# Performance work log

Hardware: AMD Instinct MI355X
Metric: run time of the kernel (lower is better)

Reference implementation:

```python
import jax, jax.numpy as jnp
import numpy as np

N_NODES = 100000
N_EDGES = 1600000
D_IN = 128
D_HID = 128
D_OUT = 128


def setup_inputs() -> dict:
    key = jax.random.key(0)
    ks = jax.random.split(key, 12)
    x = jax.random.normal(ks[0], (N_NODES, D_IN), dtype=jnp.float32)
    edge_index = jax.random.randint(ks[1], (2, N_EDGES), 0, N_NODES, dtype=jnp.int64)
    s = 0.05
    # GraphConv layer l: out = agg @ w_rel + x @ w_root + b  (lin_rel has bias, lin_root does not)
    w_rel1 = jax.random.normal(ks[2], (D_IN, D_HID), dtype=jnp.float32) * s
    w_root1 = jax.random.normal(ks[3], (D_IN, D_HID), dtype=jnp.float32) * s
    b1 = jax.random.normal(ks[4], (D_HID,), dtype=jnp.float32) * s
    w_rel2 = jax.random.normal(ks[5], (D_HID, D_HID), dtype=jnp.float32) * s
    w_root2 = jax.random.normal(ks[6], (D_HID, D_HID), dtype=jnp.float32) * s
    b2 = jax.random.normal(ks[7], (D_HID,), dtype=jnp.float32) * s
    w_rel3 = jax.random.normal(ks[8], (D_HID, D_OUT), dtype=jnp.float32) * s
    w_root3 = jax.random.normal(ks[9], (D_HID, D_OUT), dtype=jnp.float32) * s
    b3 = jax.random.normal(ks[10], (D_OUT,), dtype=jnp.float32) * s
    return {"x": x, "edge_index": edge_index,
            "w_rel1": w_rel1, "w_root1": w_root1, "b1": b1,
            "w_rel2": w_rel2, "w_root2": w_root2, "b2": b2,
            "w_rel3": w_rel3, "w_root3": w_root3, "b3": b3}


def _graph_conv(h, src, dst, w_rel, w_root, b):
    # sum-aggregate neighbor features (message = x_j, flow src -> dst),
    # then linear; identical math to PyG GraphConv with aggr='add'.
    agg = jax.ops.segment_sum(h[src], dst, num_segments=h.shape[0])
    return agg @ w_rel + h @ w_root + b


def reference(x, edge_index, w_rel1, w_root1, b1, w_rel2, w_root2, b2, w_rel3, w_root3, b3):
    src, dst = edge_index[0], edge_index[1]
    h = jax.nn.relu(_graph_conv(x, src, dst, w_rel1, w_root1, b1))
    h = jax.nn.relu(_graph_conv(h, src, dst, w_rel2, w_root2, b2))
    out = _graph_conv(h, src, dst, w_rel3, w_root3, b3)
    return out
```

## Files before the change

### kernel.cpp

```cpp
#include <hip/hip_runtime.h>
#include <hip/hip_bf16.h>
#include <stdint.h>

typedef __hip_bfloat16 bf16;
typedef __hip_bfloat162 bf162;

typedef __attribute__((ext_vector_type(8))) short short8;
typedef __attribute__((ext_vector_type(4))) float floatx4;

#define BSH   8
#define BSZ   256
#define CHUNK 8192
#define NBMAX 512


__device__ __forceinline__ float2 load2f(const bf16* __restrict__ p) {
    const unsigned int u = *(const unsigned int*)p;
    return make_float2(__uint_as_float((u & 0xffffu) << 16),
                       __uint_as_float(u & 0xffff0000u));
}


__global__ __launch_bounds__(256)
void cvt_kernel(const float* __restrict__ x, bf16* __restrict__ y, int n4) {
    int i = blockIdx.x * 256 + threadIdx.x;
    if (i < n4) {
        float4 v = ((const float4*)x)[i];
        bf162 a, b;
        a.x = __float2bfloat16(v.x); a.y = __float2bfloat16(v.y);
        b.x = __float2bfloat16(v.z); b.y = __float2bfloat16(v.w);
        ((bf162*)y)[i * 2]     = a;
        ((bf162*)y)[i * 2 + 1] = b;
    }
}

__global__ __launch_bounds__(256)
void prep_w_kernel(const float* __restrict__ wrel, const float* __restrict__ wroot,
                   bf16* __restrict__ wsw) {
    int t = blockIdx.x * 256 + threadIdx.x;
    if (t >= 4096) return;
    const int lane = t & 63;
    const int ct   = (t >> 6) & 7;
    const int kt   = t >> 9;
    const int kbase = kt * 32 + (lane >> 4) * 8;
    const int n     = ct * 16 + (lane & 15);
    bf16* q = wsw + (size_t)t * 8;
#pragma unroll
    for (int j = 0; j < 8; ++j) {
        const int k = kbase + j;
        const float v = (k < 128) ? wrel[k * 128 + n] : wroot[(k - 128) * 128 + n];
        q[j] = __float2bfloat16(v);
    }
}


__global__ __launch_bounds__(256)
void bhist_kernel(const int* __restrict__ dst, int* __restrict__ T,
                  int E, int NB, int GB) {
    __shared__ int lh[NBMAX];
    const int b = blockIdx.x;
    for (int u = threadIdx.x; u < NB; u += 256) lh[u] = 0;
    __syncthreads();
    const int beg = b * CHUNK, end = min(beg + CHUNK, E);
    for (int e = beg + threadIdx.x; e < end; e += 256)
        atomicAdd(&lh[dst[e] >> BSH], 1);
    __syncthreads();
    for (int u = threadIdx.x; u < NB; u += 256)
        T[u * GB + b] = lh[u];
}

__global__ __launch_bounds__(256)
void scan1_kernel(const int* __restrict__ deg, int* __restrict__ rp,
                  int* __restrict__ bsum, int n) {
    __shared__ int s[256];
    const int tid = threadIdx.x;
    const int i = blockIdx.x * 256 + tid;
    const int d = (i < n) ? deg[i] : 0;
    s[tid] = d;
    __syncthreads();
    for (int off = 1; off < 256; off <<= 1) {
        int u = (tid >= off) ? s[tid - off] : 0;
        __syncthreads();
        s[tid] += u;
        __syncthreads();
    }
    if (i < n) rp[i] = s[tid] - d;
    if (tid == 255) bsum[blockIdx.x] = s[255];
}

__global__ __launch_bounds__(512)
void scan2_kernel(int* __restrict__ bsum, int G) {
    __shared__ int s[512];
    const int tid = threadIdx.x;
    const int d = (tid < G) ? bsum[tid] : 0;
    s[tid] = d;
    __syncthreads();
    for (int off = 1; off < 512; off <<= 1) {
        int u = (tid >= off) ? s[tid - off] : 0;
        __syncthreads();
        s[tid] += u;
        __syncthreads();
    }
    if (tid < G) bsum[tid] = s[tid] - d;
}

__global__ __launch_bounds__(256)
void scan3_kernel(int* __restrict__ rp, const int* __restrict__ bsum, int n) {
    const int i = blockIdx.x * 256 + threadIdx.x;
    if (i < n) rp[i] += bsum[blockIdx.x];
}

__global__ __launch_bounds__(256)
void bscatter_kernel(const int* __restrict__ src, const int* __restrict__ dst,
                     const int* __restrict__ T, int* __restrict__ ebuf,
                     int E, int NB, int GB) {
    __shared__ int lofs[NBMAX];
    const int b = blockIdx.x;
    for (int u = threadIdx.x; u < NB; u += 256)
        lofs[u] = T[u * GB + b];
    __syncthreads();
    const int beg = b * CHUNK, end = min(beg + CHUNK, E);
    for (int e = beg + threadIdx.x; e < end; e += 256) {
        const int d = dst[e];
        const int u = d >> BSH;
        const int pos = atomicAdd(&lofs[u], 1);
        ebuf[pos] = (src[e] << BSH) | (d & (BSZ - 1));
    }
}

__global__ __launch_bounds__(256)
void bbuild_kernel(const int* __restrict__ T, const int* __restrict__ ebuf,
                   int* __restrict__ rp, int* __restrict__ col,
                   int E, int N, int NB, int GB) {
    __shared__ int s[256];
    __shared__ int lrank[256];
    const int u = blockIdx.x;
    const int tid = threadIdx.x;
    const int beg = T[u * GB];
    const int end = (u + 1 < NB) ? T[(u + 1) * GB] : E;

    lrank[tid] = 0;
    __syncthreads();
    for (int e = beg + tid; e < end; e += 256)
        atomicAdd(&lrank[ebuf[e] & (BSZ - 1)], 1);
    __syncthreads();
    const int cntv = lrank[tid];
    s[tid] = cntv;
    __syncthreads();
    for (int off = 1; off < 256; off <<= 1) {
        int v = (tid >= off) ? s[tid - off] : 0;
        __syncthreads();
        s[tid] += v;
        __syncthreads();
    }
    const int excl = s[tid] - cntv;
    const int node = u * BSZ + tid;
    if (node < N) rp[node] = beg + excl;
    if (u == NB - 1 && tid == 0) rp[N] = E;
    lrank[tid] = beg + excl;
    __syncthreads();
    for (int e = beg + tid; e < end; e += 256) {
        const int p = ebuf[e];
        const int pos = atomicAdd(&lrank[p & (BSZ - 1)], 1);
        col[pos] = p >> BSH;
    }
}


__global__ __launch_bounds__(256)
void agg_kernel(const bf16* __restrict__ h, const int* __restrict__ rp,
                const int* __restrict__ col, bf16* __restrict__ agg, int N) {
    const int lane = threadIdx.x & 63;
    const int wid  = threadIdx.x >> 6;
    const int node = blockIdx.x * 4 + wid;
    if (node >= N) return;
    const int beg = rp[node], end = rp[node + 1];
    const int f = lane * 2;
    float2 acc = make_float2(0.f, 0.f);
    int e = beg;
    for (; e + 8 <= end; e += 8) {
        const int s0 = col[e],     s1 = col[e + 1], s2 = col[e + 2], s3 = col[e + 3];
        const int s4 = col[e + 4], s5 = col[e + 5], s6 = col[e + 6], s7 = col[e + 7];
        const float2 a0 = load2f(h + (size_t)s0 * 128 + f);
        const float2 a1 = load2f(h + (size_t)s1 * 128 + f);
        const float2 a2 = load2f(h + (size_t)s2 * 128 + f);
        const float2 a3 = load2f(h + (size_t)s3 * 128 + f);
        const float2 a4 = load2f(h + (size_t)s4 * 128 + f);
        const float2 a5 = load2f(h + (size_t)s5 * 128 + f);
        const float2 a6 = load2f(h + (size_t)s6 * 128 + f);
        const float2 a7 = load2f(h + (size_t)s7 * 128 + f);
        acc.x += ((a0.x + a1.x) + (a2.x + a3.x)) + ((a4.x + a5.x) + (a6.x + a7.x));
        acc.y += ((a0.y + a1.y) + (a2.y + a3.y)) + ((a4.y + a5.y) + (a6.y + a7.y));
    }
    for (; e + 2 <= end; e += 2) {
        const int s0 = col[e], s1 = col[e + 1];
        const float2 a0 = load2f(h + (size_t)s0 * 128 + f);
        const float2 a1 = load2f(h + (size_t)s1 * 128 + f);
        acc.x += a0.x + a1.x;
        acc.y += a0.y + a1.y;
    }
    if (e < end) {
        const float2 a0 = load2f(h + (size_t)col[e] * 128 + f);
        acc.x += a0.x;
        acc.y += a0.y;
    }
    bf162 o;
    o.x = __float2bfloat16(acc.x);
    o.y = __float2bfloat16(acc.y);
    *(bf162*)(agg + (size_t)node * 128 + f) = o;
}


template <bool RELU, typename OT>
__global__ __launch_bounds__(256)
void mfma_gemm_kernel(const bf16* __restrict__ Aagg, const bf16* __restrict__ Hroot,
                      const bf16* __restrict__ wsw, const float* __restrict__ bias,
                      OT* __restrict__ out, int M) {
    const int tid  = threadIdx.x;
    const int lane = tid & 63;
    const int wave = tid >> 6;
    const int l15  = lane & 15;
    const int quad = lane >> 4;

    const int row_a = blockIdx.x * 64 + wave * 16 + l15;
    const bool rowok = row_a < M;

    floatx4 acc[8];
#pragma unroll
    for (int ct = 0; ct < 8; ++ct) acc[ct] = (floatx4){0.f, 0.f, 0.f, 0.f};

#pragma unroll
    for (int kt = 0; kt < 8; ++kt) {
        const bf16* Abase = (kt < 4) ? Aagg : Hroot;
        const int k0 = (kt & 3) * 32 + quad * 8;
        short8 afrag = (short8){0, 0, 0, 0, 0, 0, 0, 0};
        if (rowok) afrag = *(const short8*)(Abase + (size_t)row_a * 128 + k0);
#pragma unroll
        for (int ct = 0; ct < 8; ++ct) {
            const short8 bfrag = *(const short8*)(wsw + (size_t)((kt * 8 + ct) * 64 + lane) * 8);
            acc[ct] = __builtin_amdgcn_mfma_f32_16x16x32_bf16(afrag, bfrag, acc[ct], 0, 0, 0);
        }
    }

    const int row_o = blockIdx.x * 64 + wave * 16 + quad * 4;
#pragma unroll
    for (int ct = 0; ct < 8; ++ct) {
        const int colc = ct * 16 + l15;
        const float bv = bias[colc];
#pragma unroll
        for (int r = 0; r < 4; ++r) {
            const int row = row_o + r;
            if (row < M) {
                float v = acc[ct][r] + bv;
                if (RELU) v = fmaxf(v, 0.f);
                if constexpr (sizeof(OT) == 2)
                    ((bf16*)out)[(size_t)row * 128 + colc] = __float2bfloat16(v);
                else
                    ((float*)out)[(size_t)row * 128 + colc] = v;
            }
        }
    }
}


extern "C" void kernel_launch(void* const* d_in, const int* in_sizes, int n_in,
                              void* d_out, int out_size, void* d_ws, size_t ws_size,
                              hipStream_t stream) {
    const float* x       = (const float*)d_in[0];
    const int*   ei      = (const int*)d_in[1];
    const float* w_rel1  = (const float*)d_in[2];
    const float* w_root1 = (const float*)d_in[3];
    const float* b1      = (const float*)d_in[4];
    const float* w_rel2  = (const float*)d_in[5];
    const float* w_root2 = (const float*)d_in[6];
    const float* b2      = (const float*)d_in[7];
    const float* w_rel3  = (const float*)d_in[8];
    const float* w_root3 = (const float*)d_in[9];
    const float* b3      = (const float*)d_in[10];
    float* out = (float*)d_out;

    const int N = in_sizes[0] / 128;
    const int E = in_sizes[1] / 2;
    const int* src = ei;
    const int* dst = ei + E;

    char* w = (char*)d_ws;
    auto alloc = [&](size_t bytes) {
        char* p = w;
        w += (bytes + 255) & ~(size_t)255;
        return p;
    };
    int*  col  = (int*)alloc((size_t)E * 4);
    int*  rp   = (int*)alloc((size_t)(N + 1) * 4);
    bf16* h1   = (bf16*)alloc((size_t)N * 128 * 2);
    bf16* xbf  = (bf16*)alloc((size_t)N * 128 * 2);
    bf16* agg  = (bf16*)alloc((size_t)N * 128 * 2);
    bf16* wsw1 = (bf16*)alloc(32768 * 2);
    bf16* wsw2 = (bf16*)alloc(32768 * 2);
    bf16* wsw3 = (bf16*)alloc(32768 * 2);
    bf16* h2   = xbf;
    int*  T    = (int*)h1;
    int*  bsum = (int*)(h1 + 1024 * 1024);
    int*  ebuf = (int*)agg;

    const int NB = (N + BSZ - 1) / BSZ;
    const int GB = (E + CHUNK - 1) / CHUNK;
    const int nT = NB * GB;
    const int scanTBlocks = (nT + 255) / 256;

    const int aggBlocks  = (N + 3) / 4;
    const int gemmBlocks = (N + 63) / 64;
    const int cvtBlocks  = (N * 32 + 255) / 256;

    cvt_kernel<<<cvtBlocks, 256, 0, stream>>>(x, xbf, N * 32);
    prep_w_kernel<<<16, 256, 0, stream>>>(w_rel1, w_root1, wsw1);
    prep_w_kernel<<<16, 256, 0, stream>>>(w_rel2, w_root2, wsw2);
    prep_w_kernel<<<16, 256, 0, stream>>>(w_rel3, w_root3, wsw3);

    bhist_kernel<<<GB, 256, 0, stream>>>(dst, T, E, NB, GB);
    scan1_kernel<<<scanTBlocks, 256, 0, stream>>>(T, T, bsum, nT);
    scan2_kernel<<<1, 512, 0, stream>>>(bsum, scanTBlocks);
    scan3_kernel<<<scanTBlocks, 256, 0, stream>>>(T, bsum, nT);
    bscatter_kernel<<<GB, 256, 0, stream>>>(src, dst, T, ebuf, E, NB, GB);
    bbuild_kernel<<<NB, 256, 0, stream>>>(T, ebuf, rp, col, E, N, NB, GB);

    agg_kernel<<<aggBlocks, 256, 0, stream>>>(xbf, rp, col, agg, N);
    mfma_gemm_kernel<true, bf16><<<gemmBlocks, 256, 0, stream>>>(agg, xbf, wsw1, b1, h1, N);
    agg_kernel<<<aggBlocks, 256, 0, stream>>>(h1, rp, col, agg, N);
    mfma_gemm_kernel<true, bf16><<<gemmBlocks, 256, 0, stream>>>(agg, h1, wsw2, b2, h2, N);
    agg_kernel<<<aggBlocks, 256, 0, stream>>>(h2, rp, col, agg, N);
    mfma_gemm_kernel<false, float><<<gemmBlocks, 256, 0, stream>>>(agg, h2, wsw3, b3, out, N);
}
```

Before: 483.6 us.

## Fuse neighbor aggregation into MFMA GEMM via shared-memory tile per layer

Each GraphConv layer now gathers and sums neighbor rows for its 64-node tile straight into shared memory, then runs the MFMA GEMM from that tile and the root features. This removes the intermediate aggregation buffer write and read and three kernel launches. The weight and input conversion kernels are merged into one launch. Each wave now processes 16 nodes serially, which reduces the number of concurrent gathers in flight and the number of blocks.

```diff
diff --git a/kernel.cpp b/kernel.cpp
--- a/kernel.cpp
+++ b/kernel.cpp
@@ -20,25 +20,31 @@
                        __uint_as_float(u & 0xffff0000u));
 }
 
-
-__global__ __launch_bounds__(256)
-void cvt_kernel(const float* __restrict__ x, bf16* __restrict__ y, int n4) {
-    int i = blockIdx.x * 256 + threadIdx.x;
-    if (i < n4) {
-        float4 v = ((const float4*)x)[i];
-        bf162 a, b;
-        a.x = __float2bfloat16(v.x); a.y = __float2bfloat16(v.y);
-        b.x = __float2bfloat16(v.z); b.y = __float2bfloat16(v.w);
-        ((bf162*)y)[i * 2]     = a;
-        ((bf162*)y)[i * 2 + 1] = b;
-    }
-}
-
-__global__ __launch_bounds__(256)
-void prep_w_kernel(const float* __restrict__ wrel, const float* __restrict__ wroot,
-                   bf16* __restrict__ wsw) {
-    int t = blockIdx.x * 256 + threadIdx.x;
-    if (t >= 4096) return;
+__global__ __launch_bounds__(256)
+void prep_kernel(const float* __restrict__ x, bf16* __restrict__ y, int n4, int nCvt,
+                 const float* __restrict__ wr1, const float* __restrict__ wo1,
+                 const float* __restrict__ wr2, const float* __restrict__ wo2,
+                 const float* __restrict__ wr3, const float* __restrict__ wo3,
+                 bf16* __restrict__ w1, bf16* __restrict__ w2, bf16* __restrict__ w3) {
+    const int b = blockIdx.x;
+    if (b < nCvt) {
+        const int i = b * 256 + threadIdx.x;
+        if (i < n4) {
+            float4 v = ((const float4*)x)[i];
+            bf162 a, c;
+            a.x = __float2bfloat16(v.x); a.y = __float2bfloat16(v.y);
+            c.x = __float2bfloat16(v.z); c.y = __float2bfloat16(v.w);
+            ((bf162*)y)[i * 2]     = a;
+            ((bf162*)y)[i * 2 + 1] = c;
+        }
+        return;
+    }
+    int t = (b - nCvt) * 256 + threadIdx.x;
+    const int layer = t >> 12;
+    t &= 4095;
+    const float* wrel  = (layer == 0) ? wr1 : (layer == 1) ? wr2 : wr3;
+    const float* wroot = (layer == 0) ? wo1 : (layer == 1) ? wo2 : wo3;
+    bf16*        wsw   = (layer == 0) ? w1  : (layer == 1) ? w2  : w3;
     const int lane = t & 63;
     const int ct   = (t >> 6) & 7;
     const int kt   = t >> 9;
@@ -167,62 +173,62 @@
 }
 
 
-__global__ __launch_bounds__(256)
-void agg_kernel(const bf16* __restrict__ h, const int* __restrict__ rp,
-                const int* __restrict__ col, bf16* __restrict__ agg, int N) {
-    const int lane = threadIdx.x & 63;
-    const int wid  = threadIdx.x >> 6;
-    const int node = blockIdx.x * 4 + wid;
-    if (node >= N) return;
-    const int beg = rp[node], end = rp[node + 1];
-    const int f = lane * 2;
-    float2 acc = make_float2(0.f, 0.f);
-    int e = beg;
-    for (; e + 8 <= end; e += 8) {
-        const int s0 = col[e],     s1 = col[e + 1], s2 = col[e + 2], s3 = col[e + 3];
-        const int s4 = col[e + 4], s5 = col[e + 5], s6 = col[e + 6], s7 = col[e + 7];
-        const float2 a0 = load2f(h + (size_t)s0 * 128 + f);
-        const float2 a1 = load2f(h + (size_t)s1 * 128 + f);
-        const float2 a2 = load2f(h + (size_t)s2 * 128 + f);
-        const float2 a3 = load2f(h + (size_t)s3 * 128 + f);
-        const float2 a4 = load2f(h + (size_t)s4 * 128 + f);
-        const float2 a5 = load2f(h + (size_t)s5 * 128 + f);
-        const float2 a6 = load2f(h + (size_t)s6 * 128 + f);
-        const float2 a7 = load2f(h + (size_t)s7 * 128 + f);
-        acc.x += ((a0.x + a1.x) + (a2.x + a3.x)) + ((a4.x + a5.x) + (a6.x + a7.x));
-        acc.y += ((a0.y + a1.y) + (a2.y + a3.y)) + ((a4.y + a5.y) + (a6.y + a7.y));
-    }
-    for (; e + 2 <= end; e += 2) {
-        const int s0 = col[e], s1 = col[e + 1];
-        const float2 a0 = load2f(h + (size_t)s0 * 128 + f);
-        const float2 a1 = load2f(h + (size_t)s1 * 128 + f);
-        acc.x += a0.x + a1.x;
-        acc.y += a0.y + a1.y;
-    }
-    if (e < end) {
-        const float2 a0 = load2f(h + (size_t)col[e] * 128 + f);
-        acc.x += a0.x;
-        acc.y += a0.y;
-    }
-    bf162 o;
-    o.x = __float2bfloat16(acc.x);
-    o.y = __float2bfloat16(acc.y);
-    *(bf162*)(agg + (size_t)node * 128 + f) = o;
-}
-
-
 template <bool RELU, typename OT>
 __global__ __launch_bounds__(256)
-void mfma_gemm_kernel(const bf16* __restrict__ Aagg, const bf16* __restrict__ Hroot,
-                      const bf16* __restrict__ wsw, const float* __restrict__ bias,
-                      OT* __restrict__ out, int M) {
+void fused_layer_kernel(const bf16* __restrict__ H, const int* __restrict__ rp,
+                        const int* __restrict__ col, const bf16* __restrict__ wsw,
+                        const float* __restrict__ bias, OT* __restrict__ out, int M) {
+    __shared__ __align__(16) bf16 atile[64][136];
+
     const int tid  = threadIdx.x;
     const int lane = tid & 63;
     const int wave = tid >> 6;
     const int l15  = lane & 15;
     const int quad = lane >> 4;
-
-    const int row_a = blockIdx.x * 64 + wave * 16 + l15;
+    const int base = blockIdx.x * 64;
+
+    const int f = lane * 2;
+#pragma unroll 1
+    for (int i = 0; i < 16; ++i) {
+        const int node = base + wave * 16 + i;
+        float2 acc = make_float2(0.f, 0.f);
+        if (node < M) {
+            const int beg = rp[node], end = rp[node + 1];
+            int e = beg;
+            for (; e + 8 <= end; e += 8) {
+                const int s0 = col[e],     s1 = col[e + 1], s2 = col[e + 2], s3 = col[e + 3];
+                const int s4 = col[e + 4], s5 = col[e + 5], s6 = col[e + 6], s7 = col[e + 7];
+                const float2 a0 = load2f(H + (size_t)s0 * 128 + f);
+                const float2 a1 = load2f(H + (size_t)s1 * 128 + f);
+                const float2 a2 = load2f(H + (size_t)s2 * 128 + f);
+                const float2 a3 = load2f(H + (size_t)s3 * 128 + f);
+                const float2 a4 = load2f(H + (size_t)s4 * 128 + f);
+                const float2 a5 = load2f(H + (size_t)s5 * 128 + f);
+                const float2 a6 = load2f(H + (size_t)s6 * 128 + f);
+                const float2 a7 = load2f(H + (size_t)s7 * 128 + f);
+                acc.x += ((a0.x + a1.x) + (a2.x + a3.x)) + ((a4.x + a5.x) + (a6.x + a7.x));
+                acc.y += ((a0.y + a1.y) + (a2.y + a3.y)) + ((a4.y + a5.y) + (a6.y + a7.y));
+            }
+            for (; e + 2 <= end; e += 2) {
+                const int s0 = col[e], s1 = col[e + 1];
+                const float2 a0 = load2f(H + (size_t)s0 * 128 + f);
+                const float2 a1 = load2f(H + (size_t)s1 * 128 + f);
+                acc.x += a0.x + a1.x;
+                acc.y += a0.y + a1.y;
+            }
+            if (e < end) {
+                const float2 a0 = load2f(H + (size_t)col[e] * 128 + f);
+                acc.x += a0.x;
+                acc.y += a0.y;
+            }
+        }
+        bf162 o;
+        o.x = __float2bfloat16(acc.x);
+        o.y = __float2bfloat16(acc.y);
+        *(bf162*)&atile[wave * 16 + i][f] = o;
+    }
+
+    const int row_a = base + wave * 16 + l15;
     const bool rowok = row_a < M;
 
     floatx4 acc[8];
@@ -231,10 +237,14 @@
 
 #pragma unroll
     for (int kt = 0; kt < 8; ++kt) {
-        const bf16* Abase = (kt < 4) ? Aagg : Hroot;
         const int k0 = (kt & 3) * 32 + quad * 8;
-        short8 afrag = (short8){0, 0, 0, 0, 0, 0, 0, 0};
-        if (rowok) afrag = *(const short8*)(Abase + (size_t)row_a * 128 + k0);
+        short8 afrag;
+        if (kt < 4) {
+            afrag = *(const short8*)&atile[wave * 16 + l15][k0];
+        } else {
+            afrag = (short8){0, 0, 0, 0, 0, 0, 0, 0};
+            if (rowok) afrag = *(const short8*)(H + (size_t)row_a * 128 + k0);
+        }
 #pragma unroll
         for (int ct = 0; ct < 8; ++ct) {
             const short8 bfrag = *(const short8*)(wsw + (size_t)((kt * 8 + ct) * 64 + lane) * 8);
@@ -242,7 +252,7 @@
         }
     }
 
-    const int row_o = blockIdx.x * 64 + wave * 16 + quad * 4;
+    const int row_o = base + wave * 16 + quad * 4;
 #pragma unroll
     for (int ct = 0; ct < 8; ++ct) {
         const int colc = ct * 16 + l15;
@@ -294,28 +304,26 @@
     int*  rp   = (int*)alloc((size_t)(N + 1) * 4);
     bf16* h1   = (bf16*)alloc((size_t)N * 128 * 2);
     bf16* xbf  = (bf16*)alloc((size_t)N * 128 * 2);
-    bf16* agg  = (bf16*)alloc((size_t)N * 128 * 2);
+    int*  ebuf = (int*)alloc((size_t)E * 4);
     bf16* wsw1 = (bf16*)alloc(32768 * 2);
     bf16* wsw2 = (bf16*)alloc(32768 * 2);
     bf16* wsw3 = (bf16*)alloc(32768 * 2);
     bf16* h2   = xbf;
     int*  T    = (int*)h1;
     int*  bsum = (int*)(h1 + 1024 * 1024);
-    int*  ebuf = (int*)agg;
 
     const int NB = (N + BSZ - 1) / BSZ;
     const int GB = (E + CHUNK - 1) / CHUNK;
     const int nT = NB * GB;
     const int scanTBlocks = (nT + 255) / 256;
 
-    const int aggBlocks  = (N + 3) / 4;
-    const int gemmBlocks = (N + 63) / 64;
-    const int cvtBlocks  = (N * 32 + 255) / 256;
-
-    cvt_kernel<<<cvtBlocks, 256, 0, stream>>>(x, xbf, N * 32);
-    prep_w_kernel<<<16, 256, 0, stream>>>(w_rel1, w_root1, wsw1);
-    prep_w_kernel<<<16, 256, 0, stream>>>(w_rel2, w_root2, wsw2);
-    prep_w_kernel<<<16, 256, 0, stream>>>(w_rel3, w_root3, wsw3);
+    const int fusedBlocks = (N + 63) / 64;
+    const int cvtBlocks   = (N * 32 + 255) / 256;
+
+    prep_kernel<<<cvtBlocks + 48, 256, 0, stream>>>(
+        x, xbf, N * 32, cvtBlocks,
+        w_rel1, w_root1, w_rel2, w_root2, w_rel3, w_root3,
+        wsw1, wsw2, wsw3);
 
     bhist_kernel<<<GB, 256, 0, stream>>>(dst, T, E, NB, GB);
     scan1_kernel<<<scanTBlocks, 256, 0, stream>>>(T, T, bsum, nT);
@@ -324,10 +332,7 @@
     bscatter_kernel<<<GB, 256, 0, stream>>>(src, dst, T, ebuf, E, NB, GB);
     bbuild_kernel<<<NB, 256, 0, stream>>>(T, ebuf, rp, col, E, N, NB, GB);
 
-    agg_kernel<<<aggBlocks, 256, 0, stream>>>(xbf, rp, col, agg, N);
-    mfma_gemm_kernel<true, bf16><<<gemmBlocks, 256, 0, stream>>>(agg, xbf, wsw1, b1, h1, N);
-    agg_kernel<<<aggBlocks, 256, 0, stream>>>(h1, rp, col, agg, N);
-    mfma_gemm_kernel<true, bf16><<<gemmBlocks, 256, 0, stream>>>(agg, h1, wsw2, b2, h2, N);
-    agg_kernel<<<aggBlocks, 256, 0, stream>>>(h2, rp, col, agg, N);
-    mfma_gemm_kernel<false, float><<<gemmBlocks, 256, 0, stream>>>(agg, h2, wsw3, b3, out, N);
-}
+    fused_layer_kernel<true,  bf16 ><<<fusedBlocks, 256, 0, stream>>>(xbf, rp, col, wsw1, b1, h1,  N);
+    fused_layer_kernel<true,  bf16 ><<<fusedBlocks, 256, 0, stream>>>(h1,  rp, col, wsw2, b2, h2,  N);
+    fused_layer_kernel<false, float><<<fusedBlocks, 256, 0, stream>>>(h2,  rp, col, wsw3, b3, out, N);
+}
```

Measured after the change: 553.7 us. 1.14x slower.
